# Kernel optimization log

Hardware: AMD Instinct MI355X
Metric: run time of the kernel (lower is better)

The kernel has to match this reference:

```python
import jax, jax.numpy as jnp
import numpy as np

N_HEAD = 16
LORA_RANK = 16
ROPE_BASE = 10000.0


def _rope_cos_sin(T, D, dtype):
    # GPT-NeoX style rotate-half RoPE tables, shape [T, D]
    inv_freq = 1.0 / (ROPE_BASE ** (jnp.arange(0, D, 2, dtype=jnp.float32) / D))
    t = jnp.arange(T, dtype=jnp.float32)
    freqs = t[:, None] * inv_freq[None, :]          # [T, D/2]
    emb = jnp.concatenate([freqs, freqs], axis=-1)   # [T, D]
    return jnp.cos(emb).astype(dtype), jnp.sin(emb).astype(dtype)


def _rotate_half(x):
    x1, x2 = jnp.split(x, 2, axis=-1)
    return jnp.concatenate([-x2, x1], axis=-1)


def _apply_rope(q, k, cos, sin):
    # q,k: [B,H,T,D]; cos,sin: [T,D]
    c = cos[None, None, :, :]
    s = sin[None, None, :, :]
    return q * c + _rotate_half(q) * s, k * c + _rotate_half(k) * s


def setup_inputs() -> dict:
    key = jax.random.key(0)
    ks = jax.random.split(key, 6)
    B, T, C = 4, 1024, 2048
    r = LORA_RANK
    sc = 1.0 / np.sqrt(C)
    return {
        "x": jax.random.normal(ks[0], (B, T, C), jnp.float32),
        "qkvo_delta": jax.random.normal(ks[1], (B, 8 * r, C), jnp.float32) * 0.02,
        "Wq": jax.random.normal(ks[2], (C, C), jnp.float32) * sc,
        "Wk": jax.random.normal(ks[3], (C, C), jnp.float32) * sc,
        "Wv": jax.random.normal(ks[4], (C, C), jnp.float32) * sc,
        "Wo": jax.random.normal(ks[5], (C, C), jnp.float32) * sc,
    }


def reference(x, qkvo_delta, Wq, Wk, Wv, Wo):
    B, T, C = x.shape
    H = N_HEAD
    D = C // H

    # split LoRA deltas: each [B, r, C]
    dqA, dqB, dkA, dkB, dvA, dvB, doA, doB = jnp.split(qkvo_delta, 8, axis=1)

    def merged(W, dB, dA):
        # W [out,in] + dB^T @ dA -> [B, out, in]
        return W[None] + jnp.einsum('bro,bri->boi', dB, dA)

    def proj(inp, Wm):
        # inp @ Wm^T (per-batch merged weight)
        return jnp.einsum('bti,boi->bto', inp, Wm)

    q = proj(x, merged(Wq, dqB, dqA))
    k = proj(x, merged(Wk, dkB, dkA))
    v = proj(x, merged(Wv, dvB, dvA))

    # [B,T,C] -> [B,H,T,D]
    def heads(t):
        return t.reshape(B, T, H, D).transpose(0, 2, 1, 3)

    q, k, v = heads(q), heads(k), heads(v)

    cos, sin = _rope_cos_sin(T, D, x.dtype)
    q, k = _apply_rope(q, k, cos, sin)

    # full (non-causal) SDPA, matching is_causal=False in the source
    scale = 1.0 / np.sqrt(D)
    scores = jnp.einsum('bhtd,bhsd->bhts', q, k) * scale
    attn = jax.nn.softmax(scores, axis=-1)
    y = jnp.einsum('bhts,bhsd->bhtd', attn, v)

    y = y.transpose(0, 2, 1, 3).reshape(B, T, C)
    out = proj(y, merged(Wo, doB, doA))
    return out
```

## Files before the change

### kernel.cpp

```cpp
#include <hip/hip_runtime.h>
#include <cstdint>
#include <cstddef>

typedef __attribute__((ext_vector_type(8))) __bf16 bf8_t;
typedef __attribute__((ext_vector_type(8))) short s8_t;
typedef __attribute__((ext_vector_type(4))) short s4_t;
typedef __attribute__((ext_vector_type(4))) float f4_t;

__device__ __forceinline__ float bf2f(unsigned short h) {
  union { unsigned u; float f; } v; v.u = (unsigned)h << 16; return v.f;
}
__device__ __forceinline__ unsigned short f2bf(float f) {
  union { float f; unsigned u; } v; v.f = f;
  return (unsigned short)((v.u + 0x7FFFu + ((v.u >> 16) & 1u)) >> 16);
}

#define GL16(gp, lp) __builtin_amdgcn_global_load_lds( \
    (__attribute__((address_space(1))) void*)(gp),     \
    (__attribute__((address_space(3))) void*)(lp), 16, 0, 0)

struct ConvArgs {
  const float* src[6];
  unsigned short* dst[6];
  int n4[6];
  int thr[5];
};
__global__ void k_conv_all(ConvArgs a) {
  int blk = blockIdx.x, seg = 0;
#pragma unroll
  for (int s = 0; s < 5; ++s) seg += (blk >= a.thr[s]);
  int base = (seg == 0) ? 0 : a.thr[seg - 1];
  int i = (blk - base) * 256 + threadIdx.x;
  if (i >= a.n4[seg]) return;
  float4 v = reinterpret_cast<const float4*>(a.src[seg])[i];
  s4_t o;
  o.x = (short)f2bf(v.x); o.y = (short)f2bf(v.y);
  o.z = (short)f2bf(v.z); o.w = (short)f2bf(v.w);
  reinterpret_cast<s4_t*>(a.dst[seg])[i] = o;
}

__global__ void k_rope_table(float* __restrict__ cosT, float* __restrict__ sinT) {
  int t = blockIdx.x, d = threadIdx.x;
  float inv = exp2f(-(float)d * (13.287712379549449f / 64.0f));
  float ang = (float)t * inv;
  cosT[t * 64 + d] = cosf(ang);
  sinT[t * 64 + d] = sinf(ang);
}

#define UOFF 262144
__global__ __launch_bounds__(256) void k_lora_mfma(
    const unsigned short* __restrict__ X,
    const unsigned short* __restrict__ dlb,
    float* __restrict__ u, int pstart, int pcount) {
  __shared__ __align__(16) unsigned short Xs[64 * 64];
  __shared__ __align__(16) unsigned short Da[64 * 64];
  const int t = threadIdx.x;
  const int b = blockIdx.y;
  const int z = blockIdx.z;
  const int m0 = blockIdx.x * 64;
  const int w = t >> 6, lane = t & 63, lr = lane & 15, lg = lane >> 4;
  const int nrow = pcount * 16;
  f4_t acc[4] = {};
  for (int k0 = z * 1024; k0 < z * 1024 + 1024; k0 += 64) {
    __syncthreads();
#pragma unroll
    for (int i = 0; i < 2; ++i) {
      int idx = i * 256 + t;
      int row = idx >> 3, c = idx & 7;
      GL16(X + ((size_t)b * 1024 + m0 + row) * 2048 + k0 + ((c ^ (row & 7)) * 8),
           Xs + (size_t)idx * 8);
      int ric = row < nrow ? row : nrow - 1;
      int g = (pstart + (ric >> 4)) * 32 + (ric & 15);
      GL16(dlb + ((size_t)b * 128 + g) * 2048 + k0 + ((c ^ (ric & 7)) * 8),
           Da + (size_t)idx * 8);
    }
    __syncthreads();
#pragma unroll
    for (int kk = 0; kk < 2; ++kk) {
      bf8_t af = *(const bf8_t*)&Xs[(w * 16 + lr) * 64 + (((kk * 4 + lg) ^ (lr & 7)) * 8)];
#pragma unroll
      for (int n = 0; n < 4; ++n) {
        if (n < pcount) {
          bf8_t bfv = *(const bf8_t*)&Da[(n * 16 + lr) * 64 + (((kk * 4 + lg) ^ (lr & 7)) * 8)];
          acc[n] = __builtin_amdgcn_mfma_f32_16x16x32_bf16(af, bfv, acc[n], 0, 0, 0);
        }
      }
    }
  }
#pragma unroll
  for (int n = 0; n < 4; ++n) {
    if (n < pcount) {
#pragma unroll
      for (int j = 0; j < 4; ++j)
        u[(size_t)z * UOFF +
          (((size_t)b * 4 + pstart + n) * 16 + lr) * 1024 + m0 + w * 16 + lg * 4 + j] = acc[n][j];
    }
  }
}

struct GArgs {
  const unsigned short *Bw0, *Bw1, *Bw2;
  void *o0, *o1, *o2;
  int m0_, m1_, m2_;
  int p0_, p1_, p2_;
};
#define BM 128
#define BN 128
#define BKK 64
__global__ __launch_bounds__(256, 2) void k_gemm(
    const unsigned short* __restrict__ A,
    GArgs ga,
    const float* __restrict__ u,
    const float* __restrict__ dl) {
  constexpr int K = 2048;
  const int z = blockIdx.z;
  const unsigned short* Bw = z == 0 ? ga.Bw0 : (z == 1 ? ga.Bw1 : ga.Bw2);
  void* outv = z == 0 ? ga.o0 : (z == 1 ? ga.o1 : ga.o2);
  const int mode = z == 0 ? ga.m0_ : (z == 1 ? ga.m1_ : ga.m2_);
  const int p = z == 0 ? ga.p0_ : (z == 1 ? ga.p1_ : ga.p2_);
  __shared__ unsigned short As[BM * BKK];
  __shared__ unsigned short Bs[BN * BKK];
  const int t = threadIdx.x;
  const int m0 = blockIdx.y * BM;
  const int n0 = blockIdx.x * BN;
  const int lane = t & 63;
  const int w = t >> 6;
  const int wr = (w >> 1) * 64, wc = (w & 1) * 64;
  const int lr = lane & 15;
  const int lg = lane >> 4;
  const int srow = t >> 3;
  const int sdst = (t & 7) * 8;
  const int ssrc = ((t & 7) ^ (srow & 7)) * 8;
  f4_t acc[4][4] = {};

  for (int k0 = 0; k0 < K; k0 += BKK) {
#pragma unroll
    for (int j = 0; j < 4; ++j) {
      int row = j * 32 + srow;
      GL16(A  + (size_t)(m0 + row) * K + k0 + ssrc, As + row * BKK + sdst);
      GL16(Bw + (size_t)(n0 + row) * K + k0 + ssrc, Bs + row * BKK + sdst);
    }
    __syncthreads();
#pragma unroll
    for (int kk = 0; kk < 2; ++kk) {
      bf8_t af[4], bfr[4];
#pragma unroll
      for (int m = 0; m < 4; ++m) {
        int row_ = wr + m * 16 + lr;
        af[m] = *(const bf8_t*)&As[row_ * BKK + (((kk * 4 + lg) ^ (lr & 7)) * 8)];
      }
#pragma unroll
      for (int n = 0; n < 4; ++n) {
        int row_ = wc + n * 16 + lr;
        bfr[n] = *(const bf8_t*)&Bs[row_ * BKK + (((kk * 4 + lg) ^ (lr & 7)) * 8)];
      }
#pragma unroll
      for (int m = 0; m < 4; ++m)
#pragma unroll
        for (int n = 0; n < 4; ++n)
          acc[m][n] = __builtin_amdgcn_mfma_f32_16x16x32_bf16(af[m], bfr[n], acc[m][n], 0, 0, 0);
    }
    __syncthreads();
  }

  const int b = m0 >> 10;
  const int t0r = m0 & 1023;
  for (int idx = t; idx < 128 * 32; idx += 256) {
    int rr = idx >> 5, r = idx & 31;
    float val = 0.0f;
    if (r < 16) {
      size_t ub = (((size_t)b * 4 + p) * 16 + r) * 1024 + t0r + rr;
      val = u[ub] + u[UOFF + ub];
    }
    As[rr * 32 + r] = f2bf(val);
  }
  for (int idx = t; idx < 128 * 32; idx += 256) {
    int cc = idx >> 5, r = idx & 31;
    float val = (r < 16) ? dl[((size_t)b * 128 + p * 32 + 16 + r) * 2048 + n0 + cc] : 0.0f;
    Bs[cc * 32 + r] = f2bf(val);
  }
  __syncthreads();
  {
    bf8_t af[4], bfr[4];
#pragma unroll
    for (int m = 0; m < 4; ++m)
      af[m] = *(const bf8_t*)&As[(wr + m * 16 + lr) * 32 + lg * 8];
#pragma unroll
    for (int n = 0; n < 4; ++n)
      bfr[n] = *(const bf8_t*)&Bs[(wc + n * 16 + lr) * 32 + lg * 8];
#pragma unroll
    for (int m = 0; m < 4; ++m)
#pragma unroll
      for (int n = 0; n < 4; ++n)
        acc[m][n] = __builtin_amdgcn_mfma_f32_16x16x32_bf16(af[m], bfr[n], acc[m][n], 0, 0, 0);
  }

  unsigned short* out16 = (unsigned short*)outv;
  float* out32 = (float*)outv;
#pragma unroll
  for (int m = 0; m < 4; ++m) {
    int ri = wr + m * 16 + lg * 4;
#pragma unroll
    for (int j = 0; j < 4; ++j) {
      int grow = m0 + ri + j;
      int gb = grow >> 10, gt = grow & 1023;
#pragma unroll
      for (int n = 0; n < 4; ++n) {
        int gcol = n0 + wc + n * 16 + lr;
        float fv = acc[m][n][j];
        if (mode == 0) {
          size_t dst = (((size_t)gb * 16 + (gcol >> 7)) * 1024 + gt) * 128 + (gcol & 127);
          out16[dst] = f2bf(fv);
        } else if (mode == 1) {
          size_t dst = (((size_t)gb * 16 + (gcol >> 7)) * 128 + (gcol & 127)) * 1024 + gt;
          out16[dst] = f2bf(fv);
        } else {
          out32[(size_t)grow * 2048 + gcol] = fv;
        }
      }
    }
  }
}

__global__ void k_rope2(unsigned short* __restrict__ Xq,
                        unsigned short* __restrict__ Xk,
                        const float* __restrict__ cosT, const float* __restrict__ sinT) {
  int gb = blockIdx.x;
  unsigned short* X = (gb < 2048) ? Xq : Xk;
  int idx = (gb & 2047) * 256 + threadIdx.x;
  int d0 = (idx & 7) * 8;
  int tt = (idx >> 3) & 1023;
  size_t base = (size_t)(idx >> 3) * 128 + d0;
  s8_t a = *(s8_t*)&X[base];
  s8_t bb = *(s8_t*)&X[base + 64];
  float4 c0 = *(const float4*)&cosT[tt * 64 + d0];
  float4 c1 = *(const float4*)&cosT[tt * 64 + d0 + 4];
  float4 sv0 = *(const float4*)&sinT[tt * 64 + d0];
  float4 sv1 = *(const float4*)&sinT[tt * 64 + d0 + 4];
  float cv[8] = {c0.x, c0.y, c0.z, c0.w, c1.x, c1.y, c1.z, c1.w};
  float sw[8] = {sv0.x, sv0.y, sv0.z, sv0.w, sv1.x, sv1.y, sv1.z, sv1.w};
  s8_t ra, rb;
#pragma unroll
  for (int j = 0; j < 8; ++j) {
    float av = bf2f((unsigned short)a[j]);
    float bv = bf2f((unsigned short)bb[j]);
    ra[j] = (short)f2bf(av * cv[j] - bv * sw[j]);
    rb[j] = (short)f2bf(bv * cv[j] + av * sw[j]);
  }
  *(s8_t*)&X[base] = ra;
  *(s8_t*)&X[base + 64] = rb;
}

__global__ __launch_bounds__(512, 4) void k_attn(
    const unsigned short* __restrict__ Qg,
    const unsigned short* __restrict__ Kg,
    const unsigned short* __restrict__ Vt,
    unsigned short* __restrict__ Y) {
  const float scale = 0.08838834764831845f;
  const float L2E = 1.4426950408889634f;
  const int bid = blockIdx.x;
  const int wg = (bid & 7) * 64 + (bid >> 3);
  const int bh = wg >> 3;
  const int b = bh >> 4, h = bh & 15;
  const int t = threadIdx.x;
  const int w = t >> 6, lane = t & 63;
  const int lr = lane & 15, lg = lane >> 4;
  const int q0 = (wg & 7) * 128 + w * 16;
  const unsigned short* Q  = Qg + (size_t)bh * 131072;
  const unsigned short* Kp = Kg + (size_t)bh * 131072;
  const unsigned short* Vp = Vt + (size_t)bh * 131072;
  __shared__ __align__(16) unsigned short Ks[64 * 128];
  __shared__ __align__(16) unsigned short Vs[128 * 64];
  __shared__ __align__(16) unsigned short Ps[8][16 * 72];
  unsigned short* Pw = Ps[w];

  bf8_t qf[4];
#pragma unroll
  for (int kk = 0; kk < 4; ++kk)
    qf[kk] = *(const bf8_t*)&Q[(size_t)(q0 + lr) * 128 + kk * 32 + lg * 8];

  f4_t o[8] = {};
  float m_run = -1e30f, l_run = 0.0f;

  auto ldK = [&](int s0, int i) {
    int idx = i * 512 + t, s = idx >> 4, c = t & 15;
    return *(const s8_t*)&Kp[(size_t)(s0 + s) * 128 + ((c ^ (s & 7)) * 8)];
  };
  auto ldV = [&](int s0, int i) {
    int idx = i * 512 + t, d = idx >> 3, c = t & 7;
    return *(const s8_t*)&Vp[(size_t)d * 1024 + s0 + ((c ^ (d & 7)) * 8)];
  };
  s8_t kr0 = ldK(0, 0), kr1 = ldK(0, 1), vr0 = ldV(0, 0), vr1 = ldV(0, 1);

  for (int s0 = 0; s0 < 1024; s0 += 64) {
    __builtin_amdgcn_s_barrier();
    *(s8_t*)&Ks[((size_t)t) * 8]        = kr0;
    *(s8_t*)&Ks[((size_t)512 + t) * 8]  = kr1;
    *(s8_t*)&Vs[((size_t)t) * 8]        = vr0;
    *(s8_t*)&Vs[((size_t)512 + t) * 8]  = vr1;
    int sn = (s0 < 960) ? s0 + 64 : 0;
    kr0 = ldK(sn, 0); kr1 = ldK(sn, 1); vr0 = ldV(sn, 0); vr1 = ldV(sn, 1);
    asm volatile("s_waitcnt lgkmcnt(0)" ::: "memory");
    __builtin_amdgcn_s_barrier();

    f4_t sf[4];
#pragma unroll
    for (int ss = 0; ss < 4; ++ss) {
      f4_t c = {0.0f, 0.0f, 0.0f, 0.0f};
#pragma unroll
      for (int kk = 0; kk < 4; ++kk) {
        bf8_t kf = *(const bf8_t*)&Ks[(ss * 16 + lr) * 128 + (((kk * 4 + lg) ^ (lr & 7)) * 8)];
        c = __builtin_amdgcn_mfma_f32_16x16x32_bf16(kf, qf[kk], c, 0, 0, 0);
      }
      sf[ss] = c;
    }
    float vmax = -1e30f;
#pragma unroll
    for (int ss = 0; ss < 4; ++ss)
#pragma unroll
      for (int j = 0; j < 4; ++j) vmax = fmaxf(vmax, sf[ss][j]);
    vmax = fmaxf(vmax, __shfl_xor(vmax, 16));
    vmax = fmaxf(vmax, __shfl_xor(vmax, 32));
    float m_new = fmaxf(m_run, vmax * scale);
    float ratio = exp2f((m_run - m_new) * L2E);
    float lsum = 0.0f;
    float ps[4][4];
#pragma unroll
    for (int ss = 0; ss < 4; ++ss)
#pragma unroll
      for (int j = 0; j < 4; ++j) {
        float pv = exp2f((sf[ss][j] * scale - m_new) * L2E);
        ps[ss][j] = pv; lsum += pv;
      }
    lsum += __shfl_xor(lsum, 16);
    lsum += __shfl_xor(lsum, 32);
    l_run = l_run * ratio + lsum;
    m_run = m_new;
    float rq[4];
#pragma unroll
    for (int j = 0; j < 4; ++j) rq[j] = __shfl(ratio, lg * 4 + j);
#pragma unroll
    for (int n = 0; n < 8; ++n)
#pragma unroll
      for (int j = 0; j < 4; ++j) o[n][j] *= rq[j];
#pragma unroll
    for (int ss = 0; ss < 4; ++ss) {
      s4_t pk;
      pk.x = (short)f2bf(ps[ss][0]); pk.y = (short)f2bf(ps[ss][1]);
      pk.z = (short)f2bf(ps[ss][2]); pk.w = (short)f2bf(ps[ss][3]);
      *(s4_t*)&Pw[lr * 72 + ss * 16 + lg * 4] = pk;
    }
    bf8_t pa0 = *(const bf8_t*)&Pw[lr * 72 + lg * 8];
    bf8_t pa1 = *(const bf8_t*)&Pw[lr * 72 + 32 + lg * 8];
#pragma unroll
    for (int n = 0; n < 8; ++n) {
      int d = n * 16 + lr;
      bf8_t v0 = *(const bf8_t*)&Vs[d * 64 + (((0 + lg) ^ (lr & 7)) * 8)];
      bf8_t v1 = *(const bf8_t*)&Vs[d * 64 + (((4 + lg) ^ (lr & 7)) * 8)];
      o[n] = __builtin_amdgcn_mfma_f32_16x16x32_bf16(pa0, v0, o[n], 0, 0, 0);
      o[n] = __builtin_amdgcn_mfma_f32_16x16x32_bf16(pa1, v1, o[n], 0, 0, 0);
    }
  }

  float linv[4];
#pragma unroll
  for (int j = 0; j < 4; ++j) linv[j] = 1.0f / __shfl(l_run, lg * 4 + j);
#pragma unroll
  for (int n = 0; n < 8; ++n)
#pragma unroll
    for (int j = 0; j < 4; ++j) {
      int qg = q0 + lg * 4 + j;
      Y[((size_t)b * 1024 + qg) * 2048 + h * 128 + n * 16 + lr] =
          f2bf(o[n][j] * linv[j]);
    }
}

extern "C" void kernel_launch(void* const* d_in, const int* in_sizes, int n_in,
                              void* d_out, int out_size, void* d_ws, size_t ws_size,
                              hipStream_t stream) {
  const float* x  = (const float*)d_in[0];
  const float* dl = (const float*)d_in[1];
  const float* W[4] = {(const float*)d_in[2], (const float*)d_in[3],
                       (const float*)d_in[4], (const float*)d_in[5]};
  char* ws = (char*)d_ws;
  size_t off = 0;
  auto take = [&](size_t bytes) {
    void* p = ws + off; off += (bytes + 255) & ~(size_t)255; return p;
  };
  unsigned short* xb = (unsigned short*)take(8388608ull * 2);
  unsigned short* Wb[4];
  for (int i = 0; i < 4; ++i) Wb[i] = (unsigned short*)take(4194304ull * 2);
  unsigned short* qb = (unsigned short*)take(8388608ull * 2);
  unsigned short* kb = (unsigned short*)take(8388608ull * 2);
  unsigned short* vT = (unsigned short*)take(8388608ull * 2);
  unsigned short* y  = (unsigned short*)take(8388608ull * 2);
  float* u    = (float*)take(2ull * UOFF * 4);
  float* cosT = (float*)take(1024ull * 64 * 4);
  float* sinT = (float*)take(1024ull * 64 * 4);
  unsigned short* dlb = (unsigned short*)take(1048576ull * 2);
  if (off > ws_size) return;

  ConvArgs ca;
  ca.src[0] = x;  ca.dst[0] = xb;  ca.n4[0] = 2097152;
  for (int i = 0; i < 4; ++i) { ca.src[1 + i] = W[i]; ca.dst[1 + i] = Wb[i]; ca.n4[1 + i] = 1048576; }
  ca.src[5] = dl; ca.dst[5] = dlb; ca.n4[5] = 262144;
  ca.thr[0] = 8192; ca.thr[1] = 12288; ca.thr[2] = 16384; ca.thr[3] = 20480; ca.thr[4] = 24576;
  k_conv_all<<<25600, 256, 0, stream>>>(ca);
  k_rope_table<<<1024, 64, 0, stream>>>(cosT, sinT);
  k_lora_mfma<<<dim3(16, 4, 2), 256, 0, stream>>>(xb, dlb, u, 0, 3);

  GArgs gq;
  gq.Bw0 = Wb[0]; gq.o0 = qb;    gq.m0_ = 0; gq.p0_ = 0;
  gq.Bw1 = Wb[1]; gq.o1 = kb;    gq.m1_ = 0; gq.p1_ = 1;
  gq.Bw2 = Wb[2]; gq.o2 = vT;    gq.m2_ = 1; gq.p2_ = 2;
  k_gemm<<<dim3(16, 32, 3), 256, 0, stream>>>(xb, gq, u, dl);

  k_rope2<<<4096, 256, 0, stream>>>(qb, kb, cosT, sinT);
  k_attn<<<512, 512, 0, stream>>>(qb, kb, vT, y);
  k_lora_mfma<<<dim3(16, 4, 2), 256, 0, stream>>>(y, dlb, u, 3, 1);

  GArgs go;
  go.Bw0 = Wb[3]; go.o0 = d_out; go.m0_ = 2; go.p0_ = 3;
  go.Bw1 = Wb[3]; go.o1 = d_out; go.m1_ = 2; go.p1_ = 3;
  go.Bw2 = Wb[3]; go.o2 = d_out; go.m2_ = 2; go.p2_ = 3;
  k_gemm<<<dim3(16, 32, 1), 256, 0, stream>>>(y, go, u, dl);
}
```

Measured before the change: 329.9 us.

## Fuse Q RoPE into attention, add lazy rescale, setprio, XCD-aware GEMM tile mapping

Q RoPE moves into the attention kernel's Q fragment load, so the separate rope pass now touches only K. The online softmax skips rescaling the output accumulator unless the running max grows by more than a threshold. MFMA sections are wrapped in s_setprio, and GEMM blocks are remapped so each XCD works on a contiguous region to improve L2 reuse. The lazy rescale lets exponents exceed zero by up to 8 (in log2e-scaled units), so fp32 and bf16 P values may get larger.

```diff
diff --git a/kernel.cpp b/kernel.cpp
--- a/kernel.cpp
+++ b/kernel.cpp
@@ -121,8 +121,10 @@
   __shared__ unsigned short As[BM * BKK];
   __shared__ unsigned short Bs[BN * BKK];
   const int t = threadIdx.x;
-  const int m0 = blockIdx.y * BM;
-  const int n0 = blockIdx.x * BN;
+  const int lin = (int)blockIdx.x + ((int)blockIdx.y << 4);
+  const int xcd = lin & 7, rnk = lin >> 3;
+  const int m0 = (((xcd >> 1) << 3) | (rnk >> 3)) * BM;
+  const int n0 = (((xcd & 1) << 3) | (rnk & 7)) * BN;
   const int lane = t & 63;
   const int w = t >> 6;
   const int wr = (w >> 1) * 64, wc = (w & 1) * 64;
@@ -222,12 +224,9 @@
   }
 }
 
-__global__ void k_rope2(unsigned short* __restrict__ Xq,
-                        unsigned short* __restrict__ Xk,
-                        const float* __restrict__ cosT, const float* __restrict__ sinT) {
-  int gb = blockIdx.x;
-  unsigned short* X = (gb < 2048) ? Xq : Xk;
-  int idx = (gb & 2047) * 256 + threadIdx.x;
+__global__ void k_rope(unsigned short* __restrict__ X,
+                       const float* __restrict__ cosT, const float* __restrict__ sinT) {
+  int idx = blockIdx.x * 256 + threadIdx.x;
   int d0 = (idx & 7) * 8;
   int tt = (idx >> 3) & 1023;
   size_t base = (size_t)(idx >> 3) * 128 + d0;
@@ -255,6 +254,8 @@
     const unsigned short* __restrict__ Qg,
     const unsigned short* __restrict__ Kg,
     const unsigned short* __restrict__ Vt,
+    const float* __restrict__ cosT,
+    const float* __restrict__ sinT,
     unsigned short* __restrict__ Y) {
   const float scale = 0.08838834764831845f;
   const float L2E = 1.4426950408889634f;
@@ -275,9 +276,36 @@
   unsigned short* Pw = Ps[w];
 
   bf8_t qf[4];
-#pragma unroll
-  for (int kk = 0; kk < 4; ++kk)
-    qf[kk] = *(const bf8_t*)&Q[(size_t)(q0 + lr) * 128 + kk * 32 + lg * 8];
+  {
+    s8_t qs[4];
+#pragma unroll
+    for (int kk = 0; kk < 4; ++kk)
+      qs[kk] = *(const s8_t*)&Q[(size_t)(q0 + lr) * 128 + kk * 32 + lg * 8];
+    const float* ct = cosT + (size_t)(q0 + lr) * 64 + lg * 8;
+    const float* st = sinT + (size_t)(q0 + lr) * 64 + lg * 8;
+    float4 cl0 = *(const float4*)ct,        cl1 = *(const float4*)(ct + 4);
+    float4 ch0 = *(const float4*)(ct + 32), ch1 = *(const float4*)(ct + 36);
+    float4 sl0 = *(const float4*)st,        sl1 = *(const float4*)(st + 4);
+    float4 sh0 = *(const float4*)(st + 32), sh1 = *(const float4*)(st + 36);
+    float cl[8] = {cl0.x, cl0.y, cl0.z, cl0.w, cl1.x, cl1.y, cl1.z, cl1.w};
+    float ch[8] = {ch0.x, ch0.y, ch0.z, ch0.w, ch1.x, ch1.y, ch1.z, ch1.w};
+    float sl[8] = {sl0.x, sl0.y, sl0.z, sl0.w, sl1.x, sl1.y, sl1.z, sl1.w};
+    float sh[8] = {sh0.x, sh0.y, sh0.z, sh0.w, sh1.x, sh1.y, sh1.z, sh1.w};
+    s8_t r0, r1, r2, r3;
+#pragma unroll
+    for (int e = 0; e < 8; ++e) {
+      float x0 = bf2f((unsigned short)qs[0][e]);
+      float x1 = bf2f((unsigned short)qs[1][e]);
+      float x2 = bf2f((unsigned short)qs[2][e]);
+      float x3 = bf2f((unsigned short)qs[3][e]);
+      r0[e] = (short)f2bf(x0 * cl[e] - x2 * sl[e]);
+      r1[e] = (short)f2bf(x1 * ch[e] - x3 * sh[e]);
+      r2[e] = (short)f2bf(x2 * cl[e] + x0 * sl[e]);
+      r3[e] = (short)f2bf(x3 * ch[e] + x1 * sh[e]);
+    }
+    qf[0] = *(bf8_t*)&r0; qf[1] = *(bf8_t*)&r1;
+    qf[2] = *(bf8_t*)&r2; qf[3] = *(bf8_t*)&r3;
+  }
 
   f4_t o[8] = {};
   float m_run = -1e30f, l_run = 0.0f;
@@ -304,6 +332,7 @@
     __builtin_amdgcn_s_barrier();
 
     f4_t sf[4];
+    __builtin_amdgcn_s_setprio(1);
 #pragma unroll
     for (int ss = 0; ss < 4; ++ss) {
       f4_t c = {0.0f, 0.0f, 0.0f, 0.0f};
@@ -314,6 +343,7 @@
       }
       sf[ss] = c;
     }
+    __builtin_amdgcn_s_setprio(0);
     float vmax = -1e30f;
 #pragma unroll
     for (int ss = 0; ss < 4; ++ss)
@@ -321,28 +351,32 @@
       for (int j = 0; j < 4; ++j) vmax = fmaxf(vmax, sf[ss][j]);
     vmax = fmaxf(vmax, __shfl_xor(vmax, 16));
     vmax = fmaxf(vmax, __shfl_xor(vmax, 32));
-    float m_new = fmaxf(m_run, vmax * scale);
-    float ratio = exp2f((m_run - m_new) * L2E);
+    float pmax = vmax * scale;
+    if (!__all(pmax - m_run <= 8.0f)) {
+      float m_new = fmaxf(m_run, pmax);
+      float ratio = exp2f((m_run - m_new) * L2E);
+      l_run *= ratio;
+      float rq[4];
+#pragma unroll
+      for (int j = 0; j < 4; ++j) rq[j] = __shfl(ratio, lg * 4 + j);
+#pragma unroll
+      for (int n = 0; n < 8; ++n)
+#pragma unroll
+        for (int j = 0; j < 4; ++j) o[n][j] *= rq[j];
+      m_run = m_new;
+    }
     float lsum = 0.0f;
     float ps[4][4];
 #pragma unroll
     for (int ss = 0; ss < 4; ++ss)
 #pragma unroll
       for (int j = 0; j < 4; ++j) {
-        float pv = exp2f((sf[ss][j] * scale - m_new) * L2E);
+        float pv = exp2f((sf[ss][j] * scale - m_run) * L2E);
         ps[ss][j] = pv; lsum += pv;
       }
     lsum += __shfl_xor(lsum, 16);
     lsum += __shfl_xor(lsum, 32);
-    l_run = l_run * ratio + lsum;
-    m_run = m_new;
-    float rq[4];
-#pragma unroll
-    for (int j = 0; j < 4; ++j) rq[j] = __shfl(ratio, lg * 4 + j);
-#pragma unroll
-    for (int n = 0; n < 8; ++n)
-#pragma unroll
-      for (int j = 0; j < 4; ++j) o[n][j] *= rq[j];
+    l_run += lsum;
 #pragma unroll
     for (int ss = 0; ss < 4; ++ss) {
       s4_t pk;
@@ -352,6 +386,7 @@
     }
     bf8_t pa0 = *(const bf8_t*)&Pw[lr * 72 + lg * 8];
     bf8_t pa1 = *(const bf8_t*)&Pw[lr * 72 + 32 + lg * 8];
+    __builtin_amdgcn_s_setprio(1);
 #pragma unroll
     for (int n = 0; n < 8; ++n) {
       int d = n * 16 + lr;
@@ -360,6 +395,7 @@
       o[n] = __builtin_amdgcn_mfma_f32_16x16x32_bf16(pa0, v0, o[n], 0, 0, 0);
       o[n] = __builtin_amdgcn_mfma_f32_16x16x32_bf16(pa1, v1, o[n], 0, 0, 0);
     }
+    __builtin_amdgcn_s_setprio(0);
   }
 
   float linv[4];
@@ -415,8 +451,8 @@
   gq.Bw2 = Wb[2]; gq.o2 = vT;    gq.m2_ = 1; gq.p2_ = 2;
   k_gemm<<<dim3(16, 32, 3), 256, 0, stream>>>(xb, gq, u, dl);
 
-  k_rope2<<<4096, 256, 0, stream>>>(qb, kb, cosT, sinT);
-  k_attn<<<512, 512, 0, stream>>>(qb, kb, vT, y);
+  k_rope<<<2048, 256, 0, stream>>>(kb, cosT, sinT);
+  k_attn<<<512, 512, 0, stream>>>(qb, kb, vT, cosT, sinT, y);
   k_lora_mfma<<<dim3(16, 4, 2), 256, 0, stream>>>(y, dlb, u, 3, 1);
 
   GArgs go;
```

New measurement: 312.3 us. -5.3%, faster.
